# Kernel tuning notes

Hardware: AMD Instinct MI355X
Metric: run time of the kernel (lower is better)

## Reference

```python
import jax, jax.numpy as jnp
import numpy as np

# YOLOv1 loss constants (match init_kwargs)
S, B, C = 14, 2, 20
LAMBDA_COORD, LAMBDA_NOOBJ = 5.0, 0.5
BATCH = 4096


def setup_inputs() -> dict:
    key = jax.random.key(0)
    k1, k2, k3, k4, k5 = jax.random.split(key, 5)
    N = 5 * B + C
    # predictions must be positive (torch.sqrt on w,h)
    pred = jax.random.uniform(k1, (BATCH, S, S, N), jnp.float32, 1e-3, 1.0)
    # build target exactly like convert_to_yolo_format: obj cells carry the
    # same (x,y,w,h,1) in every one of the B box slots + one-hot class;
    # empty cells are all zeros (so target[...,4]==0 is the noobj mask).
    obj = (jax.random.uniform(k2, (BATCH, S, S)) < 0.3).astype(jnp.float32)
    xy = jax.random.uniform(k3, (BATCH, S, S, 2))            # cell-relative center
    wh = jax.random.uniform(k4, (BATCH, S, S, 2), minval=0.05, maxval=0.95)
    box = jnp.concatenate([xy, wh, obj[..., None]], -1) * obj[..., None]  # [Bt,S,S,5]
    boxes = jnp.tile(box, (1, 1, 1, B))                       # [Bt,S,S,5B]
    labels = jax.random.randint(k5, (BATCH, S, S), 0, C)
    cls = jax.nn.one_hot(labels, C, dtype=jnp.float32) * obj[..., None]
    target = jnp.concatenate([boxes, cls], -1)                # [Bt,S,S,5B+C]
    return {"pred": pred, "target": target}


def _to_xyxy(box):
    # torch: xyxy[:, :2] = xy/S - 0.5*wh ; xyxy[:, 2:4] = xy/S + 0.5*wh
    c = box[..., :2] / S
    h = 0.5 * box[..., 2:4]
    return jnp.concatenate([c - h, c + h], -1)


def _yolo_loss(pred, target):
    bs = pred.shape[0]
    obj = target[..., 4] > 0                                  # [Bt,S,S] coord_mask
    pb = pred[..., :5 * B].reshape(pred.shape[:-1] + (B, 5))  # [Bt,S,S,B,5]
    tb = target[..., :5 * B].reshape(target.shape[:-1] + (B, 5))
    t0 = tb[..., 0, :]                                        # torch uses bbox_target[i] (first box)

    # IoU of each of the B predicted boxes against the cell's target box
    p4 = _to_xyxy(pb)                                         # [Bt,S,S,B,4]
    t4 = _to_xyxy(t0)[..., None, :]                           # [Bt,S,S,1,4]
    lt = jnp.maximum(p4[..., :2], t4[..., :2])
    rb = jnp.minimum(p4[..., 2:], t4[..., 2:])
    whi = jnp.clip(rb - lt, 0.0)
    inter = whi[..., 0] * whi[..., 1]
    area_p = (p4[..., 2] - p4[..., 0]) * (p4[..., 3] - p4[..., 1])
    area_t = (t4[..., 2] - t4[..., 0]) * (t4[..., 3] - t4[..., 1])
    # torch stores max_iou via .item() -> detached constant target
    iou = jax.lax.stop_gradient(inter / (area_p + area_t - inter))  # [Bt,S,S,B]
    max_iou = iou.max(-1)
    idx = iou.argmax(-1)
    resp = (idx[..., None] == jnp.arange(B)) & obj[..., None]       # responsible box mask

    rf = resp.astype(pred.dtype)
    of = obj.astype(pred.dtype)
    nf = 1.0 - of

    # coord losses (responsible boxes only)
    loss_xy = jnp.sum(rf[..., None] * (pb[..., :2] - tb[..., :2]) ** 2)
    pwh = jnp.where(resp[..., None], pb[..., 2:4], 1.0)  # safe sqrt outside mask
    twh = jnp.where(resp[..., None], tb[..., 2:4], 1.0)
    loss_wh = jnp.sum(rf[..., None] * (jnp.sqrt(pwh) - jnp.sqrt(twh)) ** 2)
    # objectness: pred conf vs (detached) max IoU
    loss_obj = jnp.sum(rf * (pb[..., 4] - max_iou[..., None]) ** 2)
    # no-object: conf channels of every box slot in empty cells
    loss_noobj = jnp.sum(nf[..., None] * (pb[..., 4] - tb[..., 4]) ** 2)
    # class loss over object cells
    loss_cls = jnp.sum(of[..., None] * (pred[..., 5 * B:] - target[..., 5 * B:]) ** 2)

    loss = (LAMBDA_COORD * (loss_xy + loss_wh) + loss_obj
            + LAMBDA_NOOBJ * loss_noobj + loss_cls) / bs
    return loss


def reference(pred, target):
    return _yolo_loss(pred, target)
```

## Files before the change

### kernel.cpp

```cpp
#include <hip/hip_runtime.h>


__global__ void zero_out_kernel(float* out) { out[0] = 0.0f; }

__global__ __launch_bounds__(256) void yolo_loss_kernel(
    const float* __restrict__ pred, const float* __restrict__ target,
    float* __restrict__ out)
{
    __shared__ float sp[4][1920];
    __shared__ float st[4][1920];

    const int lane = threadIdx.x & 63;
    const int wid  = threadIdx.x >> 6;
    const size_t tile0 = ((size_t)blockIdx.x * 4 + wid) * 64;
    const float* gp = pred   + tile0 * 30;
    const float* gt = target + tile0 * 30;

    float4 rp4[7], rt4[7];
    const float4* gp4 = (const float4*)gp;
    const float4* gt4 = (const float4*)gt;
    #pragma unroll
    for (int i = 0; i < 7; ++i) {
        rp4[i] = gp4[i*64 + lane];
        rt4[i] = gt4[i*64 + lane];
    }
    float2 rp2 = ((const float2*)gp)[896 + lane];
    float2 rt2 = ((const float2*)gt)[896 + lane];

    float4* wp4 = (float4*)sp[wid];
    float4* wt4 = (float4*)st[wid];
    #pragma unroll
    for (int i = 0; i < 7; ++i) {
        wp4[i*64 + lane] = rp4[i];
        wt4[i*64 + lane] = rt4[i];
    }
    ((float2*)sp[wid])[896 + lane] = rp2;
    ((float2*)st[wid])[896 + lane] = rt2;

    float pv[30], tv[30];
    const float2* rp = (const float2*)&sp[wid][lane * 30];
    const float2* rt = (const float2*)&st[wid][lane * 30];
    #pragma unroll
    for (int j = 0; j < 15; ++j) {
        float2 a = rp[j]; pv[2*j] = a.x; pv[2*j+1] = a.y;
        float2 b = rt[j]; tv[2*j] = b.x; tv[2*j+1] = b.y;
    }

    const float invS = 1.0f / 14.0f;
    const bool obj = tv[4] > 0.0f;

    float tcx = tv[0] * invS, tcy = tv[1] * invS;
    float thw = 0.5f * tv[2], thh = 0.5f * tv[3];
    float tx1 = tcx - thw, ty1 = tcy - thh;
    float tx2 = tcx + thw, ty2 = tcy + thh;
    float area_t = (tx2 - tx1) * (ty2 - ty1);

    float iou0 = 0.0f, iou1 = 0.0f;
    #pragma unroll
    for (int b = 0; b < 2; ++b) {
        float cx = pv[5*b + 0] * invS, cy = pv[5*b + 1] * invS;
        float hw = 0.5f * pv[5*b + 2], hh = 0.5f * pv[5*b + 3];
        float x1 = cx - hw, y1 = cy - hh, x2 = cx + hw, y2 = cy + hh;
        float lx = fmaxf(x1, tx1), ly = fmaxf(y1, ty1);
        float rx = fminf(x2, tx2), ry = fminf(y2, ty2);
        float w = fmaxf(rx - lx, 0.0f), h = fmaxf(ry - ly, 0.0f);
        float inter = w * h;
        float area_p = (x2 - x1) * (y2 - y1);
        float iou = inter / (area_p + area_t - inter);
        if (b == 0) iou0 = iou; else iou1 = iou;
    }
    const bool  sel     = iou1 > iou0;
    const float max_iou = fmaxf(iou0, iou1);

    float local;
    if (obj) {
        float pbx = sel ? pv[5] : pv[0];
        float pby = sel ? pv[6] : pv[1];
        float pbw = sel ? pv[7] : pv[2];
        float pbh = sel ? pv[8] : pv[3];
        float pbc = sel ? pv[9] : pv[4];

        float dx = pbx - tv[0], dy = pby - tv[1];
        float loss_xy = dx*dx + dy*dy;

        float sw = sqrtf(pbw) - sqrtf(tv[2]);
        float sh = sqrtf(pbh) - sqrtf(tv[3]);
        float loss_wh = sw*sw + sh*sh;

        float dob = pbc - max_iou;
        float loss_obj = dob * dob;

        float loss_cls = 0.0f;
        #pragma unroll
        for (int c = 0; c < 20; ++c) {
            float d = pv[10 + c] - tv[10 + c];
            loss_cls = fmaf(d, d, loss_cls);
        }
        local = 5.0f * (loss_xy + loss_wh) + loss_obj + loss_cls;
    } else {
        float d0 = pv[4] - tv[4];
        float d1 = pv[9] - tv[9];
        local = 0.5f * (d0*d0 + d1*d1);
    }

    #pragma unroll
    for (int off = 32; off > 0; off >>= 1)
        local += __shfl_down(local, off, 64);

    __shared__ float wsum[4];
    if (lane == 0) wsum[wid] = local;
    __syncthreads();
    if (threadIdx.x == 0) {
        float s = wsum[0] + wsum[1] + wsum[2] + wsum[3];
        atomicAdd(out, s * (1.0f / 4096.0f));
    }
}

extern "C" void kernel_launch(void* const* d_in, const int* in_sizes, int n_in,
                              void* d_out, int out_size, void* d_ws, size_t ws_size,
                              hipStream_t stream) {
    const float* pred   = (const float*)d_in[0];
    const float* target = (const float*)d_in[1];
    float* out = (float*)d_out;

    zero_out_kernel<<<1, 1, 0, stream>>>(out);
    yolo_loss_kernel<<<3136, 256, 0, stream>>>(pred, target, out);
}
```

Baseline: 201.9 us.

## Stage tiles via direct global-to-LDS loads with a single reused buffer

Replaces the register round-trip (global load, then LDS store) with `__builtin_amdgcn_global_load_lds` DMA-style loads straight into shared memory. Pred and target tiles now share one LDS buffer: pred is loaded and read into registers, then target is loaded into the same space. This halves shared memory per block and raises the launch-bounds occupancy hint to 5 blocks, aiming for more waves in flight on a memory-bound kernel. The cost is that the pred and target loads are now serialized within each wave, which lowers per-wave memory-level parallelism.

```diff
diff --git a/kernel.cpp b/kernel.cpp
--- a/kernel.cpp
+++ b/kernel.cpp
@@ -3,47 +3,63 @@
 
 __global__ void zero_out_kernel(float* out) { out[0] = 0.0f; }
 
-__global__ __launch_bounds__(256) void yolo_loss_kernel(
+__device__ __forceinline__ void gll16(const void* g, void* l) {
+    __builtin_amdgcn_global_load_lds(
+        (const __attribute__((address_space(1))) void*)(uintptr_t)g,
+        (__attribute__((address_space(3))) void*)(uintptr_t)l, 16, 0, 0);
+}
+__device__ __forceinline__ void gll4(const void* g, void* l) {
+    __builtin_amdgcn_global_load_lds(
+        (const __attribute__((address_space(1))) void*)(uintptr_t)g,
+        (__attribute__((address_space(3))) void*)(uintptr_t)l, 4, 0, 0);
+}
+
+__device__ __forceinline__ void stage_tile(const float* __restrict__ g,
+                                           float* lds, int lane)
+{
+    const char* gb = (const char*)g;
+    char* lb = (char*)lds;
+    #pragma unroll
+    for (int i = 0; i < 7; ++i)
+        gll16(gb + i * 1024 + lane * 16, lb + i * 1024);
+    gll4(gb + 7168 + lane * 4, lb + 7168);
+    gll4(gb + 7424 + lane * 4, lb + 7424);
+}
+
+__global__ __launch_bounds__(256, 5) void yolo_loss_kernel(
     const float* __restrict__ pred, const float* __restrict__ target,
     float* __restrict__ out)
 {
-    __shared__ float sp[4][1920];
-    __shared__ float st[4][1920];
+    __shared__ __align__(16) float sbuf[4][1920];
 
     const int lane = threadIdx.x & 63;
     const int wid  = threadIdx.x >> 6;
     const size_t tile0 = ((size_t)blockIdx.x * 4 + wid) * 64;
     const float* gp = pred   + tile0 * 30;
     const float* gt = target + tile0 * 30;
-
-    float4 rp4[7], rt4[7];
-    const float4* gp4 = (const float4*)gp;
-    const float4* gt4 = (const float4*)gt;
-    #pragma unroll
-    for (int i = 0; i < 7; ++i) {
-        rp4[i] = gp4[i*64 + lane];
-        rt4[i] = gt4[i*64 + lane];
-    }
-    float2 rp2 = ((const float2*)gp)[896 + lane];
-    float2 rt2 = ((const float2*)gt)[896 + lane];
-
-    float4* wp4 = (float4*)sp[wid];
-    float4* wt4 = (float4*)st[wid];
-    #pragma unroll
-    for (int i = 0; i < 7; ++i) {
-        wp4[i*64 + lane] = rp4[i];
-        wt4[i*64 + lane] = rt4[i];
-    }
-    ((float2*)sp[wid])[896 + lane] = rp2;
-    ((float2*)st[wid])[896 + lane] = rt2;
+    float* sw = sbuf[wid];
 
     float pv[30], tv[30];
-    const float2* rp = (const float2*)&sp[wid][lane * 30];
-    const float2* rt = (const float2*)&st[wid][lane * 30];
-    #pragma unroll
-    for (int j = 0; j < 15; ++j) {
-        float2 a = rp[j]; pv[2*j] = a.x; pv[2*j+1] = a.y;
-        float2 b = rt[j]; tv[2*j] = b.x; tv[2*j+1] = b.y;
+
+    stage_tile(gp, sw, lane);
+    asm volatile("s_waitcnt vmcnt(0)" ::: "memory");
+    {
+        const float2* rp = (const float2*)&sw[lane * 30];
+        #pragma unroll
+        for (int j = 0; j < 15; ++j) {
+            float2 a = rp[j]; pv[2*j] = a.x; pv[2*j+1] = a.y;
+        }
+    }
+    asm volatile("s_waitcnt lgkmcnt(0)" ::: "memory");
+
+    stage_tile(gt, sw, lane);
+    asm volatile("s_waitcnt vmcnt(0)" ::: "memory");
+    {
+        const float2* rt = (const float2*)&sw[lane * 30];
+        #pragma unroll
+        for (int j = 0; j < 15; ++j) {
+            float2 b = rt[j]; tv[2*j] = b.x; tv[2*j+1] = b.y;
+        }
     }
 
     const float invS = 1.0f / 14.0f;
@@ -83,9 +99,9 @@
         float dx = pbx - tv[0], dy = pby - tv[1];
         float loss_xy = dx*dx + dy*dy;
 
-        float sw = sqrtf(pbw) - sqrtf(tv[2]);
-        float sh = sqrtf(pbh) - sqrtf(tv[3]);
-        float loss_wh = sw*sw + sh*sh;
+        float sw_ = sqrtf(pbw) - sqrtf(tv[2]);
+        float sh_ = sqrtf(pbh) - sqrtf(tv[3]);
+        float loss_wh = sw_*sw_ + sh_*sh_;
 
         float dob = pbc - max_iou;
         float loss_obj = dob * dob;
```

New measurement: 204.0 us. Within noise of the previous version (+1.1%).
